# Kernel tuning notes

Hardware: AMD Instinct MI355X
Metric: run time of the kernel (lower is better)

## Reference

```python
import jax, jax.numpy as jnp
import numpy as np

N_HEAD = 16

def setup_inputs() -> dict:
    key = jax.random.key(0)
    k1, k2, k3 = jax.random.split(key, 3)
    B, S, D = 2, 2048, 1024
    x = jax.random.normal(k1, (B, S, D), dtype=jnp.float32)
    w_attn = jax.random.normal(k2, (D, 3 * D), dtype=jnp.float32) * 0.02
    b_attn = jnp.zeros((3 * D,), dtype=jnp.float32)
    w_proj = jax.random.normal(k3, (D, D), dtype=jnp.float32) * 0.02
    b_proj = jnp.zeros((D,), dtype=jnp.float32)
    return {"x": x, "w_attn": w_attn, "b_attn": b_attn, "w_proj": w_proj, "b_proj": b_proj}

def reference(x, w_attn, b_attn, w_proj, b_proj):
    B, S, D = x.shape
    hd = D // N_HEAD
    qkv = x @ w_attn + b_attn                      # [B,S,3D]
    q, k, v = jnp.split(qkv, 3, axis=-1)
    def heads(t):  # [B,S,D] -> [B,H,S,hd]
        return t.reshape(B, S, N_HEAD, hd).transpose(0, 2, 1, 3)
    q, k, v = heads(q), heads(k), heads(v)
    # NOTE: original forward applies NO scaling and NO causal mask; dropout=eval (identity)
    scores = jnp.einsum('bhqd,bhkd->bhqk', q, k)   # [B,H,S,S]
    probs = jax.nn.softmax(scores, axis=-1)
    out = jnp.einsum('bhqk,bhkd->bhqd', probs, v)  # [B,H,S,hd]
    out = out.transpose(0, 2, 1, 3).reshape(B, S, D)
    return out @ w_proj + b_proj
```

## Files before the change

### kernel.cpp

```cpp
#include <hip/hip_runtime.h>

typedef _Float16 f16;
typedef _Float16 f16x8 __attribute__((ext_vector_type(8)));
typedef _Float16 f16x4 __attribute__((ext_vector_type(4)));
typedef float    f32x4 __attribute__((ext_vector_type(4)));
typedef unsigned int u32;
typedef unsigned int u32x4 __attribute__((ext_vector_type(4)));

#define LOG2E 1.44269504088896340736f
#define EXPC  (13.0f * 1.44269504088896340736f)

__device__ __forceinline__ void gload_lds16(const void* g, void* l) {
  __builtin_amdgcn_global_load_lds(
      (const __attribute__((address_space(1))) void*)g,
      (__attribute__((address_space(3))) void*)l, 16, 0, 0);
}

__device__ __forceinline__ void block_sync() {
  asm volatile("" ::: "memory");
  __builtin_amdgcn_s_barrier();
  asm volatile("" ::: "memory");
}

__global__ void k_cast_x(const float* __restrict__ in, f16* __restrict__ out) {
  int i = blockIdx.x * blockDim.x + threadIdx.x;
  f32x4 v = ((const f32x4*)in)[i];
  f16x4 o;
  o[0] = (f16)v[0]; o[1] = (f16)v[1]; o[2] = (f16)v[2]; o[3] = (f16)v[3];
  ((f16x4*)out)[i] = o;
}

__global__ void k_transpose_cast(const float* __restrict__ in, f16* __restrict__ out,
                                 int R, int C) {
  __shared__ float tile[32][33];
  int c0 = blockIdx.x * 32, r0 = blockIdx.y * 32;
  int tx = threadIdx.x, ty = threadIdx.y;
#pragma unroll
  for (int i = 0; i < 4; i++)
    tile[ty + i * 8][tx] = in[(size_t)(r0 + ty + i * 8) * C + c0 + tx];
  __syncthreads();
#pragma unroll
  for (int i = 0; i < 4; i++)
    out[(size_t)(c0 + ty + i * 8) * R + r0 + tx] = (f16)tile[tx][ty + i * 8];
}

template <int EPI>
__global__ __launch_bounds__(256)
void k_gemm(const f16* __restrict__ A, const f16* __restrict__ BT,
            const float* __restrict__ bias,
            f16* __restrict__ out_qk, f16* __restrict__ out_vT,
            float* __restrict__ out_f) {
  constexpr int K = 1024;
  __shared__ f16 smem[4][128 * 64];
  const int t = threadIdx.x;
  const int l = t & 63;
  const int w = t >> 6;
  const int wm = (w >> 1) * 64;
  const int wn = (w & 1) * 64;
  const int m0 = blockIdx.x * 128;
  const int n0 = blockIdx.y * 128;
  const int lr = l & 15;
  const int lk = (l >> 4) * 8;

  const f16* Ap = A + (size_t)(m0 + (t >> 3)) * K + ((t & 7) << 3);
  const f16* Bp = BT + (size_t)(n0 + (t >> 3)) * K + ((t & 7) << 3);

#define GSTAGE(buf) do { \
    _Pragma("unroll") \
    for (int i2 = 0; i2 < 4; i2++) \
      gload_lds16(Ap + (size_t)(i2 * 32) * K, &smem[buf][(i2 * 256 + t) * 8]); \
    _Pragma("unroll") \
    for (int i2 = 0; i2 < 4; i2++) \
      gload_lds16(Bp + (size_t)(i2 * 32) * K, &smem[2 + buf][(i2 * 256 + t) * 8]); \
    Ap += 64; Bp += 64; } while (0)

  f32x4 acc[4][4] = {};

#define GCOMPUTE(buf) do { \
    _Pragma("unroll") \
    for (int kk = 0; kk < 64; kk += 32) { \
      f16x8 af[4], bf[4]; \
      _Pragma("unroll") \
      for (int i = 0; i < 4; i++) \
        af[i] = *(const f16x8*)&smem[buf][(wm + i * 16 + lr) * 64 + kk + lk]; \
      _Pragma("unroll") \
      for (int j = 0; j < 4; j++) \
        bf[j] = *(const f16x8*)&smem[2 + buf][(wn + j * 16 + lr) * 64 + kk + lk]; \
      _Pragma("unroll") \
      for (int i = 0; i < 4; i++) \
        _Pragma("unroll") \
        for (int j = 0; j < 4; j++) \
          acc[i][j] = __builtin_amdgcn_mfma_f32_16x16x32_f16(af[i], bf[j], acc[i][j], 0, 0, 0); \
    } } while (0)

  GSTAGE(0);
  asm volatile("s_waitcnt vmcnt(0)" ::: "memory");
  block_sync();

  for (int kt = 0; kt < 16; kt += 2) {
    GSTAGE(1);
    GCOMPUTE(0);
    asm volatile("s_waitcnt vmcnt(0)" ::: "memory");
    block_sync();
    if (kt + 2 < 16) GSTAGE(0);
    GCOMPUTE(1);
    asm volatile("s_waitcnt vmcnt(0)" ::: "memory");
    block_sync();
  }
#undef GSTAGE
#undef GCOMPUTE

  if (EPI == 1) {
#pragma unroll
    for (int i = 0; i < 4; i++) {
      int mbase = m0 + wm + i * 16 + (l >> 4) * 4;
#pragma unroll
      for (int j = 0; j < 4; j++) {
        int n = n0 + wn + j * 16 + lr;
        float bv = bias[n];
#pragma unroll
        for (int r = 0; r < 4; r++)
          out_f[(size_t)(mbase + r) * 1024 + n] = acc[i][j][r] + bv;
      }
    }
  } else if (n0 < 2048) {
#pragma unroll
    for (int i = 0; i < 4; i++) {
      int mbase = m0 + wm + i * 16 + (l >> 4) * 4;
#pragma unroll
      for (int j = 0; j < 4; j++) {
        int n = n0 + wn + j * 16 + lr;
        float bv = bias[n];
        float sc = (n0 + wn + j * 16 < 1024) ? LOG2E : 1.0f;
#pragma unroll
        for (int r = 0; r < 4; r++)
          out_qk[(size_t)(mbase + r) * 2048 + n] = (f16)((acc[i][j][r] + bv) * sc);
      }
    }
  } else {
    f16* scr = &smem[0][0];
#pragma unroll
    for (int i = 0; i < 4; i++) {
      int s0 = wm + i * 16 + (l >> 4) * 4;
#pragma unroll
      for (int j = 0; j < 4; j++) {
        int nl = wn + j * 16 + lr;
        float bv = bias[n0 + nl];
        f16x4 pv;
#pragma unroll
        for (int r = 0; r < 4; r++) pv[r] = (f16)(acc[i][j][r] + bv);
        *(f16x4*)&scr[nl * 128 + (s0 ^ ((nl & 15) << 3))] = pv;
      }
    }
    block_sync();
    const int b = m0 >> 11;
    const int sbase = m0 & 2047;
#pragma unroll
    for (int p = 0; p < 8; p++) {
      int nl = (t >> 4) + p * 16;
      int sc = (t & 15) << 3;
      f16x8 vv = *(const f16x8*)&scr[nl * 128 + (sc ^ ((nl & 15) << 3))];
      int ng = (n0 - 2048) + nl;
      int hg = ng >> 6, d = ng & 63;
      *(f16x8*)&out_vT[(((size_t)(b * 16 + hg) * 64 + d) << 11) + sbase + sc] = vv;
    }
  }
}

__global__ __launch_bounds__(256, 4)
void k_attn(const f16* __restrict__ qk, const f16* __restrict__ vT,
            f16* __restrict__ aout) {
  __shared__ f16 Kl[2][64 * 64];
  __shared__ f16 Vl[2][64 * 64];
  const int t = threadIdx.x;
  const int l = t & 63;
  const int w = t >> 6;
  const int lr = l & 15;
  const int lg = l >> 4;
  const int lk = lg * 8;

  const int o  = (blockIdx.x & 7) * 128 + (blockIdx.x >> 3);
  const int qt = o & 31;
  const int bh = o >> 5;
  const int b  = bh >> 4;
  const int h  = bh & 15;
  const int q0 = qt * 64 + w * 16;

  const f16* qp = qk + (size_t)(b * 2048 + q0 + lr) * 2048 + h * 64 + lk;
  f16x8 qf0 = *(const f16x8*)qp;
  f16x8 qf1 = *(const f16x8*)(qp + 32);

  const f16* kg = qk + (size_t)(b * 2048) * 2048 + 1024 + h * 64;
  const f16* vg = vT + (size_t)(bh * 64) * 2048;
  const int row8 = t >> 3;
  const int off0 = row8 * 2048 + (((t & 7) ^ (row8 & 7)) << 3);
  const int off1 = off0 + 32 * 2048;

#define STAGE(B) do { \
    gload_lds16(kg + off0, &Kl[B][t * 8]); \
    gload_lds16(kg + off1, &Kl[B][(256 + t) * 8]); \
    gload_lds16(vg + off0, &Vl[B][t * 8]); \
    gload_lds16(vg + off1, &Vl[B][(256 + t) * 8]); \
    kg += 64 * 2048; vg += 64; } while (0)

  f32x4 oa[4] = {};
  f32x4 ssum = {};
  const f32x4 initc = {-EXPC, -EXPC, -EXPC, -EXPC};
  f16x8 ones;
#pragma unroll
  for (int j = 0; j < 8; j++) ones[j] = (f16)1.0f;

  STAGE(0);
  asm volatile("s_waitcnt vmcnt(0)" ::: "memory");
  block_sync();

#define TILE_BODY(B) do { \
    f32x4 sa[4]; \
    __builtin_amdgcn_s_setprio(1); \
    _Pragma("unroll") \
    for (int c = 0; c < 4; c++) { \
      const int ks = c >> 1, cc = c & 1; \
      const int row = ks * 32 + (lr >> 2) * 8 + (lr & 3) * 2 + cc; \
      const int r7 = row & 7; \
      f16x8 kf0 = *(const f16x8*)&Kl[B][(row * 8 + (lg ^ r7)) * 8]; \
      f16x8 kf1 = *(const f16x8*)&Kl[B][(row * 8 + ((lg + 4) ^ r7)) * 8]; \
      sa[c] = __builtin_amdgcn_mfma_f32_16x16x32_f16(kf0, qf0, initc, 0, 0, 0); \
      sa[c] = __builtin_amdgcn_mfma_f32_16x16x32_f16(kf1, qf1, sa[c], 0, 0, 0); \
    } \
    __builtin_amdgcn_s_setprio(0); \
    _Pragma("unroll") \
    for (int c = 0; c < 4; c++) \
      _Pragma("unroll") \
      for (int r = 0; r < 4; r++) \
        sa[c][r] = exp2f(sa[c][r]); \
    u32 pka[2][4]; \
    _Pragma("unroll") \
    for (int ks = 0; ks < 2; ks++) \
      _Pragma("unroll") \
      for (int u = 0; u < 4; u++) \
        pka[ks][u] = __builtin_bit_cast(u32, \
            __builtin_amdgcn_cvt_pkrtz(sa[2 * ks][u], sa[2 * ks + 1][u])); \
    f16x8 pa0 = __builtin_bit_cast(f16x8, (u32x4){pka[0][0], pka[0][1], pka[0][2], pka[0][3]}); \
    f16x8 pa1 = __builtin_bit_cast(f16x8, (u32x4){pka[1][0], pka[1][1], pka[1][2], pka[1][3]}); \
    __builtin_amdgcn_s_setprio(1); \
    ssum = __builtin_amdgcn_mfma_f32_16x16x32_f16(pa0, ones, ssum, 0, 0, 0); \
    ssum = __builtin_amdgcn_mfma_f32_16x16x32_f16(pa1, ones, ssum, 0, 0, 0); \
    _Pragma("unroll") \
    for (int c4 = 0; c4 < 4; c4++) { \
      const int row = c4 * 16 + lr; \
      const int r7 = row & 7; \
      f16x8 vf0 = *(const f16x8*)&Vl[B][(row * 8 + (lg ^ r7)) * 8]; \
      f16x8 vf1 = *(const f16x8*)&Vl[B][(row * 8 + ((lg + 4) ^ r7)) * 8]; \
      oa[c4] = __builtin_amdgcn_mfma_f32_16x16x32_f16(pa0, vf0, oa[c4], 0, 0, 0); \
      oa[c4] = __builtin_amdgcn_mfma_f32_16x16x32_f16(pa1, vf1, oa[c4], 0, 0, 0); \
    } \
    __builtin_amdgcn_s_setprio(0); \
    asm volatile("s_waitcnt vmcnt(0)" ::: "memory"); \
    block_sync(); } while (0)

  for (int tt = 0; tt < 32; tt += 2) {
    STAGE(1);
    TILE_BODY(0);
    if (tt + 2 < 32) STAGE(0);
    TILE_BODY(1);
  }
#undef STAGE
#undef TILE_BODY

#pragma unroll
  for (int r = 0; r < 4; r++) {
    float ia = 1.0f / ssum[r];
    size_t rowa = (size_t)(b * 2048 + q0 + lg * 4 + r);
#pragma unroll
    for (int c4 = 0; c4 < 4; c4++)
      aout[rowa * 1024 + h * 64 + c4 * 16 + lr] = (f16)(oa[c4][r] * ia);
  }
}

extern "C" void kernel_launch(void* const* d_in, const int* in_sizes, int n_in,
                              void* d_out, int out_size, void* d_ws, size_t ws_size,
                              hipStream_t stream) {
  const float* x      = (const float*)d_in[0];
  const float* w_attn = (const float*)d_in[1];
  const float* b_attn = (const float*)d_in[2];
  const float* w_proj = (const float*)d_in[3];
  const float* b_proj = (const float*)d_in[4];
  float* out = (float*)d_out;

  char* p = (char*)d_ws;
  f16* xh  = (f16*)p;  p += (size_t)4096 * 1024 * 2;
  f16* waT = (f16*)p;  p += (size_t)3072 * 1024 * 2;
  f16* wpT = (f16*)p;  p += (size_t)1024 * 1024 * 2;
  f16* qkb = (f16*)p;  p += (size_t)4096 * 2048 * 2;
  f16* vTb = (f16*)p;  p += (size_t)32 * 64 * 2048 * 2;
  f16* aob = (f16*)p;  p += (size_t)4096 * 1024 * 2;
  if ((size_t)(p - (char*)d_ws) > ws_size) return;

  k_cast_x<<<4096, 256, 0, stream>>>(x, xh);
  k_transpose_cast<<<dim3(96, 32), dim3(32, 8), 0, stream>>>(w_attn, waT, 1024, 3072);
  k_transpose_cast<<<dim3(32, 32), dim3(32, 8), 0, stream>>>(w_proj, wpT, 1024, 1024);
  k_gemm<0><<<dim3(32, 24), 256, 0, stream>>>(xh, waT, b_attn, qkb, vTb, nullptr);
  k_attn<<<1024, 256, 0, stream>>>(qkb, vTb, aob);
  k_gemm<1><<<dim3(32, 8), 256, 0, stream>>>(aob, wpT, b_proj, nullptr, nullptr, out);
}
```

Before: 126.9 us.

## Process two 16-row query groups per wave in attention to reuse K/V fragments

Each wave now handles 32 query rows (two 16-row MFMA groups) instead of 16, so each K/V tile loaded from LDS feeds twice as many MFMAs and total K/V global traffic is halved. The grid shrinks from 1024 to 512 blocks and launch bounds drop to 2 blocks per CU to make room for the doubled accumulator registers. The LDS swizzle also gains an extra XOR term on the row's upper bits, intended to cut bank conflicts. The cost is higher register pressure, lower occupancy and fewer blocks to spread across CUs.

New measurement: 125.7 us. Within noise of the previous version (-1.0%).

```diff
diff --git a/kernel.cpp b/kernel.cpp
--- a/kernel.cpp
+++ b/kernel.cpp
@@ -167,7 +167,7 @@
   }
 }
 
-__global__ __launch_bounds__(256, 4)
+__global__ __launch_bounds__(256, 2)
 void k_attn(const f16* __restrict__ qk, const f16* __restrict__ vT,
             f16* __restrict__ aout) {
   __shared__ f16 Kl[2][64 * 64];
@@ -179,22 +179,26 @@
   const int lg = l >> 4;
   const int lk = lg * 8;
 
-  const int o  = (blockIdx.x & 7) * 128 + (blockIdx.x >> 3);
-  const int qt = o & 31;
-  const int bh = o >> 5;
+  const int o  = (blockIdx.x & 7) * 64 + (blockIdx.x >> 3);
+  const int qt = o & 15;
+  const int bh = o >> 4;
   const int b  = bh >> 4;
   const int h  = bh & 15;
-  const int q0 = qt * 64 + w * 16;
-
-  const f16* qp = qk + (size_t)(b * 2048 + q0 + lr) * 2048 + h * 64 + lk;
-  f16x8 qf0 = *(const f16x8*)qp;
-  f16x8 qf1 = *(const f16x8*)(qp + 32);
+  const int q0 = qt * 128 + w * 32;
+
+  const f16* qp0 = qk + (size_t)(b * 2048 + q0 + lr) * 2048 + h * 64 + lk;
+  const f16* qp1 = qp0 + (size_t)16 * 2048;
+  f16x8 qf0 = *(const f16x8*)qp0;
+  f16x8 qf1 = *(const f16x8*)(qp0 + 32);
+  f16x8 qg0 = *(const f16x8*)qp1;
+  f16x8 qg1 = *(const f16x8*)(qp1 + 32);
 
   const f16* kg = qk + (size_t)(b * 2048) * 2048 + 1024 + h * 64;
   const f16* vg = vT + (size_t)(bh * 64) * 2048;
   const int row8 = t >> 3;
-  const int off0 = row8 * 2048 + (((t & 7) ^ (row8 & 7)) << 3);
-  const int off1 = off0 + 32 * 2048;
+  const int sc0 = (t & 7) ^ (row8 & 7) ^ (row8 >> 3);
+  const int off0 = row8 * 2048 + sc0 * 8;
+  const int off1 = (row8 + 32) * 2048 + (sc0 ^ 4) * 8;
 
 #define STAGE(B) do { \
     gload_lds16(kg + off0, &Kl[B][t * 8]); \
@@ -203,8 +207,8 @@
     gload_lds16(vg + off1, &Vl[B][(256 + t) * 8]); \
     kg += 64 * 2048; vg += 64; } while (0)
 
-  f32x4 oa[4] = {};
-  f32x4 ssum = {};
+  f32x4 oa[4] = {}, ob[4] = {};
+  f32x4 ssa = {}, ssb = {};
   const f32x4 initc = {-EXPC, -EXPC, -EXPC, -EXPC};
   f16x8 ones;
 #pragma unroll
@@ -215,44 +219,57 @@
   block_sync();
 
 #define TILE_BODY(B) do { \
-    f32x4 sa[4]; \
+    f32x4 sa[4], sb[4]; \
     __builtin_amdgcn_s_setprio(1); \
     _Pragma("unroll") \
     for (int c = 0; c < 4; c++) { \
       const int ks = c >> 1, cc = c & 1; \
       const int row = ks * 32 + (lr >> 2) * 8 + (lr & 3) * 2 + cc; \
-      const int r7 = row & 7; \
-      f16x8 kf0 = *(const f16x8*)&Kl[B][(row * 8 + (lg ^ r7)) * 8]; \
-      f16x8 kf1 = *(const f16x8*)&Kl[B][(row * 8 + ((lg + 4) ^ r7)) * 8]; \
+      const int fr = (row & 7) ^ (row >> 3); \
+      f16x8 kf0 = *(const f16x8*)&Kl[B][(row * 8 + (lg ^ fr)) * 8]; \
+      f16x8 kf1 = *(const f16x8*)&Kl[B][(row * 8 + ((lg + 4) ^ fr)) * 8]; \
       sa[c] = __builtin_amdgcn_mfma_f32_16x16x32_f16(kf0, qf0, initc, 0, 0, 0); \
       sa[c] = __builtin_amdgcn_mfma_f32_16x16x32_f16(kf1, qf1, sa[c], 0, 0, 0); \
+      sb[c] = __builtin_amdgcn_mfma_f32_16x16x32_f16(kf0, qg0, initc, 0, 0, 0); \
+      sb[c] = __builtin_amdgcn_mfma_f32_16x16x32_f16(kf1, qg1, sb[c], 0, 0, 0); \
     } \
     __builtin_amdgcn_s_setprio(0); \
     _Pragma("unroll") \
     for (int c = 0; c < 4; c++) \
       _Pragma("unroll") \
-      for (int r = 0; r < 4; r++) \
+      for (int r = 0; r < 4; r++) { \
         sa[c][r] = exp2f(sa[c][r]); \
-    u32 pka[2][4]; \
+        sb[c][r] = exp2f(sb[c][r]); \
+      } \
+    u32 pka[2][4], pkb[2][4]; \
     _Pragma("unroll") \
     for (int ks = 0; ks < 2; ks++) \
       _Pragma("unroll") \
-      for (int u = 0; u < 4; u++) \
+      for (int u = 0; u < 4; u++) { \
         pka[ks][u] = __builtin_bit_cast(u32, \
             __builtin_amdgcn_cvt_pkrtz(sa[2 * ks][u], sa[2 * ks + 1][u])); \
+        pkb[ks][u] = __builtin_bit_cast(u32, \
+            __builtin_amdgcn_cvt_pkrtz(sb[2 * ks][u], sb[2 * ks + 1][u])); \
+      } \
     f16x8 pa0 = __builtin_bit_cast(f16x8, (u32x4){pka[0][0], pka[0][1], pka[0][2], pka[0][3]}); \
     f16x8 pa1 = __builtin_bit_cast(f16x8, (u32x4){pka[1][0], pka[1][1], pka[1][2], pka[1][3]}); \
+    f16x8 pb0 = __builtin_bit_cast(f16x8, (u32x4){pkb[0][0], pkb[0][1], pkb[0][2], pkb[0][3]}); \
+    f16x8 pb1 = __builtin_bit_cast(f16x8, (u32x4){pkb[1][0], pkb[1][1], pkb[1][2], pkb[1][3]}); \
     __builtin_amdgcn_s_setprio(1); \
-    ssum = __builtin_amdgcn_mfma_f32_16x16x32_f16(pa0, ones, ssum, 0, 0, 0); \
-    ssum = __builtin_amdgcn_mfma_f32_16x16x32_f16(pa1, ones, ssum, 0, 0, 0); \
+    ssa = __builtin_amdgcn_mfma_f32_16x16x32_f16(pa0, ones, ssa, 0, 0, 0); \
+    ssa = __builtin_amdgcn_mfma_f32_16x16x32_f16(pa1, ones, ssa, 0, 0, 0); \
+    ssb = __builtin_amdgcn_mfma_f32_16x16x32_f16(pb0, ones, ssb, 0, 0, 0); \
+    ssb = __builtin_amdgcn_mfma_f32_16x16x32_f16(pb1, ones, ssb, 0, 0, 0); \
     _Pragma("unroll") \
     for (int c4 = 0; c4 < 4; c4++) { \
       const int row = c4 * 16 + lr; \
-      const int r7 = row & 7; \
-      f16x8 vf0 = *(const f16x8*)&Vl[B][(row * 8 + (lg ^ r7)) * 8]; \
-      f16x8 vf1 = *(const f16x8*)&Vl[B][(row * 8 + ((lg + 4) ^ r7)) * 8]; \
+      const int fr = (row & 7) ^ (row >> 3); \
+      f16x8 vf0 = *(const f16x8*)&Vl[B][(row * 8 + (lg ^ fr)) * 8]; \
+      f16x8 vf1 = *(const f16x8*)&Vl[B][(row * 8 + ((lg + 4) ^ fr)) * 8]; \
       oa[c4] = __builtin_amdgcn_mfma_f32_16x16x32_f16(pa0, vf0, oa[c4], 0, 0, 0); \
       oa[c4] = __builtin_amdgcn_mfma_f32_16x16x32_f16(pa1, vf1, oa[c4], 0, 0, 0); \
+      ob[c4] = __builtin_amdgcn_mfma_f32_16x16x32_f16(pb0, vf0, ob[c4], 0, 0, 0); \
+      ob[c4] = __builtin_amdgcn_mfma_f32_16x16x32_f16(pb1, vf1, ob[c4], 0, 0, 0); \
     } \
     __builtin_amdgcn_s_setprio(0); \
     asm volatile("s_waitcnt vmcnt(0)" ::: "memory"); \
@@ -269,11 +286,15 @@
 
 #pragma unroll
   for (int r = 0; r < 4; r++) {
-    float ia = 1.0f / ssum[r];
+    float ia = 1.0f / ssa[r];
+    float ib = 1.0f / ssb[r];
     size_t rowa = (size_t)(b * 2048 + q0 + lg * 4 + r);
-#pragma unroll
-    for (int c4 = 0; c4 < 4; c4++)
+    size_t rowb = rowa + 16;
+#pragma unroll
+    for (int c4 = 0; c4 < 4; c4++) {
       aout[rowa * 1024 + h * 64 + c4 * 16 + lr] = (f16)(oa[c4][r] * ia);
+      aout[rowb * 1024 + h * 64 + c4 * 16 + lr] = (f16)(ob[c4][r] * ib);
+    }
   }
 }
 
@@ -300,6 +321,6 @@
   k_transpose_cast<<<dim3(96, 32), dim3(32, 8), 0, stream>>>(w_attn, waT, 1024, 3072);
   k_transpose_cast<<<dim3(32, 32), dim3(32, 8), 0, stream>>>(w_proj, wpT, 1024, 1024);
   k_gemm<0><<<dim3(32, 24), 256, 0, stream>>>(xh, waT, b_attn, qkb, vTb, nullptr);
-  k_attn<<<1024, 256, 0, stream>>>(qkb, vTb, aob);
+  k_attn<<<512, 256, 0, stream>>>(qkb, vTb, aob);
   k_gemm<1><<<dim3(32, 8), 256, 0, stream>>>(aob, wpT, b_proj, nullptr, nullptr, out);
 }
```

## Triple-buffer attention K/V loads and swizzle GEMM LDS tiles against bank conflicts

Applied to the files above, without the earlier changes.

The attention kernel moves from a double buffer to a three-stage LDS ring. Loads are issued two tiles ahead and waited on with a partial vmcnt, so global-load latency overlaps more compute. The K/V swizzle gains an extra XOR term, and the GEMM LDS tiles get an XOR swizzle to cut bank conflicts on fragment reads. The cost is more LDS per block and launch bounds lowered from 4 to 3 blocks per SM, which reduces occupancy.

Result: no change. 129.4 us (+1.9%).

```diff
diff --git a/kernel.cpp b/kernel.cpp
--- a/kernel.cpp
+++ b/kernel.cpp
@@ -60,10 +60,13 @@
   const int m0 = blockIdx.x * 128;
   const int n0 = blockIdx.y * 128;
   const int lr = l & 15;
-  const int lk = (l >> 4) * 8;
-
-  const f16* Ap = A + (size_t)(m0 + (t >> 3)) * K + ((t & 7) << 3);
-  const f16* Bp = BT + (size_t)(n0 + (t >> 3)) * K + ((t & 7) << 3);
+  const int lg = l >> 4;
+  const int fr8 = lr & 7;
+
+  const int row8g = t >> 3;
+  const int scg = (t & 7) ^ (row8g & 7);
+  const f16* Ap = A + (size_t)(m0 + row8g) * K + scg * 8;
+  const f16* Bp = BT + (size_t)(n0 + row8g) * K + scg * 8;
 
 #define GSTAGE(buf) do { \
     _Pragma("unroll") \
@@ -79,13 +82,14 @@
 #define GCOMPUTE(buf) do { \
     _Pragma("unroll") \
     for (int kk = 0; kk < 64; kk += 32) { \
+      const int cbase = (kk >> 3) + lg;   \
       f16x8 af[4], bf[4]; \
       _Pragma("unroll") \
       for (int i = 0; i < 4; i++) \
-        af[i] = *(const f16x8*)&smem[buf][(wm + i * 16 + lr) * 64 + kk + lk]; \
+        af[i] = *(const f16x8*)&smem[buf][((wm + i * 16 + lr) * 8 + (cbase ^ fr8)) * 8]; \
       _Pragma("unroll") \
       for (int j = 0; j < 4; j++) \
-        bf[j] = *(const f16x8*)&smem[2 + buf][(wn + j * 16 + lr) * 64 + kk + lk]; \
+        bf[j] = *(const f16x8*)&smem[2 + buf][((wn + j * 16 + lr) * 8 + (cbase ^ fr8)) * 8]; \
       _Pragma("unroll") \
       for (int i = 0; i < 4; i++) \
         _Pragma("unroll") \
@@ -167,11 +171,11 @@
   }
 }
 
-__global__ __launch_bounds__(256, 4)
+__global__ __launch_bounds__(256, 3)
 void k_attn(const f16* __restrict__ qk, const f16* __restrict__ vT,
             f16* __restrict__ aout) {
-  __shared__ f16 Kl[2][64 * 64];
-  __shared__ f16 Vl[2][64 * 64];
+  __shared__ f16 Kl[3][64 * 64];
+  __shared__ f16 Vl[3][64 * 64];
   const int t = threadIdx.x;
   const int l = t & 63;
   const int w = t >> 6;
@@ -193,8 +197,9 @@
   const f16* kg = qk + (size_t)(b * 2048) * 2048 + 1024 + h * 64;
   const f16* vg = vT + (size_t)(bh * 64) * 2048;
   const int row8 = t >> 3;
-  const int off0 = row8 * 2048 + (((t & 7) ^ (row8 & 7)) << 3);
-  const int off1 = off0 + 32 * 2048;
+  const int sc0 = (t & 7) ^ (row8 & 7) ^ (row8 >> 3);
+  const int off0 = row8 * 2048 + sc0 * 8;
+  const int off1 = (row8 + 32) * 2048 + (sc0 ^ 4) * 8;
 
 #define STAGE(B) do { \
     gload_lds16(kg + off0, &Kl[B][t * 8]); \
@@ -210,10 +215,6 @@
 #pragma unroll
   for (int j = 0; j < 8; j++) ones[j] = (f16)1.0f;
 
-  STAGE(0);
-  asm volatile("s_waitcnt vmcnt(0)" ::: "memory");
-  block_sync();
-
 #define TILE_BODY(B) do { \
     f32x4 sa[4]; \
     __builtin_amdgcn_s_setprio(1); \
@@ -221,9 +222,9 @@
     for (int c = 0; c < 4; c++) { \
       const int ks = c >> 1, cc = c & 1; \
       const int row = ks * 32 + (lr >> 2) * 8 + (lr & 3) * 2 + cc; \
-      const int r7 = row & 7; \
-      f16x8 kf0 = *(const f16x8*)&Kl[B][(row * 8 + (lg ^ r7)) * 8]; \
-      f16x8 kf1 = *(const f16x8*)&Kl[B][(row * 8 + ((lg + 4) ^ r7)) * 8]; \
+      const int fr = (row & 7) ^ (row >> 3); \
+      f16x8 kf0 = *(const f16x8*)&Kl[B][(row * 8 + (lg ^ fr)) * 8]; \
+      f16x8 kf1 = *(const f16x8*)&Kl[B][(row * 8 + ((lg + 4) ^ fr)) * 8]; \
       sa[c] = __builtin_amdgcn_mfma_f32_16x16x32_f16(kf0, qf0, initc, 0, 0, 0); \
       sa[c] = __builtin_amdgcn_mfma_f32_16x16x32_f16(kf1, qf1, sa[c], 0, 0, 0); \
     } \
@@ -248,24 +249,41 @@
     _Pragma("unroll") \
     for (int c4 = 0; c4 < 4; c4++) { \
       const int row = c4 * 16 + lr; \
-      const int r7 = row & 7; \
-      f16x8 vf0 = *(const f16x8*)&Vl[B][(row * 8 + (lg ^ r7)) * 8]; \
-      f16x8 vf1 = *(const f16x8*)&Vl[B][(row * 8 + ((lg + 4) ^ r7)) * 8]; \
+      const int fr = (row & 7) ^ (row >> 3); \
+      f16x8 vf0 = *(const f16x8*)&Vl[B][(row * 8 + (lg ^ fr)) * 8]; \
+      f16x8 vf1 = *(const f16x8*)&Vl[B][(row * 8 + ((lg + 4) ^ fr)) * 8]; \
       oa[c4] = __builtin_amdgcn_mfma_f32_16x16x32_f16(pa0, vf0, oa[c4], 0, 0, 0); \
       oa[c4] = __builtin_amdgcn_mfma_f32_16x16x32_f16(pa1, vf1, oa[c4], 0, 0, 0); \
     } \
-    __builtin_amdgcn_s_setprio(0); \
-    asm volatile("s_waitcnt vmcnt(0)" ::: "memory"); \
+    __builtin_amdgcn_s_setprio(0); } while (0)
+
+#define PHASE(RD, WR) do { \
+    STAGE(WR); \
+    asm volatile("s_waitcnt vmcnt(8)" ::: "memory"); \
+    __builtin_amdgcn_sched_barrier(0); \
+    block_sync(); \
+    TILE_BODY(RD); \
     block_sync(); } while (0)
 
-  for (int tt = 0; tt < 32; tt += 2) {
-    STAGE(1);
-    TILE_BODY(0);
-    if (tt + 2 < 32) STAGE(0);
-    TILE_BODY(1);
+  STAGE(0);
+  STAGE(1);
+  for (int it = 0; it < 10; ++it) {
+    PHASE(0, 2);
+    PHASE(1, 0);
+    PHASE(2, 1);
   }
+  asm volatile("s_waitcnt vmcnt(4)" ::: "memory");
+  __builtin_amdgcn_sched_barrier(0);
+  block_sync();
+  TILE_BODY(0);
+  block_sync();
+  asm volatile("s_waitcnt vmcnt(0)" ::: "memory");
+  __builtin_amdgcn_sched_barrier(0);
+  block_sync();
+  TILE_BODY(1);
 #undef STAGE
 #undef TILE_BODY
+#undef PHASE
 
 #pragma unroll
   for (int r = 0; r < 4; r++) {
```

## Swizzle GEMM LDS tiles and load attention V fragments directly from global

Applied to the files above, without the earlier changes.

The GEMM kernel now writes its LDS tiles with an XOR swizzle of the 16-byte chunk index and reads them back the same way, to avoid LDS bank conflicts on the MFMA fragment loads. In the attention kernel, V no longer goes through LDS. Each wave loads its V fragments straight from global memory into registers at the start of each tile, which halves LDS traffic and footprint. In exchange, every wave now fetches V redundantly from global/L2, and the tile ends with a vmcnt(0) wait on those loads, which may expose their latency.

Result: slower. 190.8 us (+50.3%).

```diff
diff --git a/kernel.cpp b/kernel.cpp
--- a/kernel.cpp
+++ b/kernel.cpp
@@ -60,10 +60,13 @@
   const int m0 = blockIdx.x * 128;
   const int n0 = blockIdx.y * 128;
   const int lr = l & 15;
-  const int lk = (l >> 4) * 8;
-
-  const f16* Ap = A + (size_t)(m0 + (t >> 3)) * K + ((t & 7) << 3);
-  const f16* Bp = BT + (size_t)(n0 + (t >> 3)) * K + ((t & 7) << 3);
+  const int lg = l >> 4;
+  const int fr8 = lr & 7;
+
+  const int row8g = t >> 3;
+  const int scg = (t & 7) ^ (row8g & 7);
+  const f16* Ap = A + (size_t)(m0 + row8g) * K + scg * 8;
+  const f16* Bp = BT + (size_t)(n0 + row8g) * K + scg * 8;
 
 #define GSTAGE(buf) do { \
     _Pragma("unroll") \
@@ -79,13 +82,14 @@
 #define GCOMPUTE(buf) do { \
     _Pragma("unroll") \
     for (int kk = 0; kk < 64; kk += 32) { \
+      const int cbase = (kk >> 3) + lg;   \
       f16x8 af[4], bf[4]; \
       _Pragma("unroll") \
       for (int i = 0; i < 4; i++) \
-        af[i] = *(const f16x8*)&smem[buf][(wm + i * 16 + lr) * 64 + kk + lk]; \
+        af[i] = *(const f16x8*)&smem[buf][((wm + i * 16 + lr) * 8 + (cbase ^ fr8)) * 8]; \
       _Pragma("unroll") \
       for (int j = 0; j < 4; j++) \
-        bf[j] = *(const f16x8*)&smem[2 + buf][(wn + j * 16 + lr) * 64 + kk + lk]; \
+        bf[j] = *(const f16x8*)&smem[2 + buf][((wn + j * 16 + lr) * 8 + (cbase ^ fr8)) * 8]; \
       _Pragma("unroll") \
       for (int i = 0; i < 4; i++) \
         _Pragma("unroll") \
@@ -171,7 +175,6 @@
 void k_attn(const f16* __restrict__ qk, const f16* __restrict__ vT,
             f16* __restrict__ aout) {
   __shared__ f16 Kl[2][64 * 64];
-  __shared__ f16 Vl[2][64 * 64];
   const int t = threadIdx.x;
   const int l = t & 63;
   const int w = t >> 6;
@@ -191,17 +194,16 @@
   f16x8 qf1 = *(const f16x8*)(qp + 32);
 
   const f16* kg = qk + (size_t)(b * 2048) * 2048 + 1024 + h * 64;
-  const f16* vg = vT + (size_t)(bh * 64) * 2048;
   const int row8 = t >> 3;
   const int off0 = row8 * 2048 + (((t & 7) ^ (row8 & 7)) << 3);
   const int off1 = off0 + 32 * 2048;
 
+  const f16* vgd = vT + ((size_t)(bh * 64) + lr) * 2048 + lk;
+
 #define STAGE(B) do { \
     gload_lds16(kg + off0, &Kl[B][t * 8]); \
     gload_lds16(kg + off1, &Kl[B][(256 + t) * 8]); \
-    gload_lds16(vg + off0, &Vl[B][t * 8]); \
-    gload_lds16(vg + off1, &Vl[B][(256 + t) * 8]); \
-    kg += 64 * 2048; vg += 64; } while (0)
+    kg += 64 * 2048; } while (0)
 
   f32x4 oa[4] = {};
   f32x4 ssum = {};
@@ -215,6 +217,13 @@
   block_sync();
 
 #define TILE_BODY(B) do { \
+     \
+    f16x8 vfr[4][2]; \
+    _Pragma("unroll") \
+    for (int c4 = 0; c4 < 4; c4++) \
+      _Pragma("unroll") \
+      for (int ks = 0; ks < 2; ks++) \
+        vfr[c4][ks] = *(const f16x8*)(vgd + (size_t)(c4 * 16) * 2048 + ks * 32); \
     f32x4 sa[4]; \
     __builtin_amdgcn_s_setprio(1); \
     _Pragma("unroll") \
@@ -247,14 +256,11 @@
     ssum = __builtin_amdgcn_mfma_f32_16x16x32_f16(pa1, ones, ssum, 0, 0, 0); \
     _Pragma("unroll") \
     for (int c4 = 0; c4 < 4; c4++) { \
-      const int row = c4 * 16 + lr; \
-      const int r7 = row & 7; \
-      f16x8 vf0 = *(const f16x8*)&Vl[B][(row * 8 + (lg ^ r7)) * 8]; \
-      f16x8 vf1 = *(const f16x8*)&Vl[B][(row * 8 + ((lg + 4) ^ r7)) * 8]; \
-      oa[c4] = __builtin_amdgcn_mfma_f32_16x16x32_f16(pa0, vf0, oa[c4], 0, 0, 0); \
-      oa[c4] = __builtin_amdgcn_mfma_f32_16x16x32_f16(pa1, vf1, oa[c4], 0, 0, 0); \
+      oa[c4] = __builtin_amdgcn_mfma_f32_16x16x32_f16(pa0, vfr[c4][0], oa[c4], 0, 0, 0); \
+      oa[c4] = __builtin_amdgcn_mfma_f32_16x16x32_f16(pa1, vfr[c4][1], oa[c4], 0, 0, 0); \
     } \
     __builtin_amdgcn_s_setprio(0); \
+    vgd += 64; \
     asm volatile("s_waitcnt vmcnt(0)" ::: "memory"); \
     block_sync(); } while (0)
 
```
